# Optimization experiments

Hardware: AMD Instinct MI355X
Metric: run time of the kernel (lower is better)

Reference implementation:

```python
import jax, jax.numpy as jnp
import numpy as np

B, S, D, H = 4, 2048, 1024, 16
DH = D // H
SCALE = 1.0 / np.sqrt(DH).astype(np.float32)


def setup_inputs() -> dict:
    key = jax.random.key(0)
    k1, k2, k3 = jax.random.split(key, 3)
    x = jax.random.normal(k1, (B, S, D), dtype=jnp.float32)
    w_qkv = jax.random.normal(k2, (D, 3 * D), dtype=jnp.float32) * (1.0 / np.sqrt(D))
    b_qkv = jnp.zeros((3 * D,), dtype=jnp.float32)
    w_out = jax.random.normal(k3, (D, D), dtype=jnp.float32) * (1.0 / np.sqrt(D))
    b_out = jnp.zeros((D,), dtype=jnp.float32)
    return {"x": x, "w_qkv": w_qkv, "b_qkv": b_qkv, "w_out": w_out, "b_out": b_out}


def reference(x, w_qkv, b_qkv, w_out, b_out):
    b, s, d = x.shape
    qkv = x @ w_qkv + b_qkv                       # [b, s, 3d]
    qkv = qkv.reshape(b, s, 3, H, DH)
    qkv = jnp.transpose(qkv, (2, 0, 3, 1, 4))     # [3, b, h, s, dh]
    q, k, v = qkv[0], qkv[1], qkv[2]
    scores = jnp.einsum("bhqd,bhkd->bhqk", q, k) * SCALE
    weights = jax.nn.softmax(scores, axis=-1)
    attn = jnp.einsum("bhqk,bhkd->bhqd", weights, v)
    attn = jnp.transpose(attn, (0, 2, 1, 3)).reshape(b, s, d)
    return attn @ w_out + b_out
```

## Files before the change

kernel.cpp:

```cpp
#include <hip/hip_runtime.h>


typedef _Float16 f16;
typedef __attribute__((ext_vector_type(8))) _Float16 f16x8;
typedef __attribute__((ext_vector_type(4))) _Float16 f16x4;
typedef __attribute__((ext_vector_type(4))) float f32x4;
typedef __attribute__((ext_vector_type(16))) float f32x16;
typedef __attribute__((ext_vector_type(4))) unsigned u32x4;
typedef __attribute__((ext_vector_type(2))) int i32x2;

#define MFMA16F(a, b, c) __builtin_amdgcn_mfma_f32_16x16x32_f16((a), (b), (c), 0, 0, 0)
#define MFMA32F(a, b, c) __builtin_amdgcn_mfma_f32_32x32x16_f16((a), (b), (c), 0, 0, 0)

__device__ __forceinline__ i32x2 pl32_swap(unsigned a, unsigned b) {
  return __builtin_amdgcn_permlane32_swap((int)a, (int)b, false, false);
}

__device__ __forceinline__ void gload16(void* lds, const void* g) {
  __builtin_amdgcn_global_load_lds(
      (const __attribute__((address_space(1))) unsigned int*)g,
      (__attribute__((address_space(3))) unsigned int*)lds, 16, 0, 0);
}

__device__ __forceinline__ f16* lds_addr(f16* t, int row, int col) {
  return (f16*)((char*)t + row * 128 + ((col * 2) ^ ((row & 7) << 4)));
}
__device__ __forceinline__ f16x8 lds8(const f16* t, int row, int col) {
  return *(const f16x8*)lds_addr((f16*)t, row, col);
}

#define Q_PRESCALE 0.18033688011117f

__device__ __forceinline__ void transpose_tile(const float* __restrict__ in,
                                               f16* __restrict__ t_out, int R, int C,
                                               int bx, int by, int tid,
                                               float (*tile)[65]) {
  const int r0 = by * 64;
  const int c0 = bx * 64;
  const int lr = tid >> 4;
  const int lc = (tid & 15) * 4;
#pragma unroll
  for (int i = 0; i < 4; ++i) {
    float4 v = *(const float4*)&in[(size_t)(r0 + lr + i * 16) * C + c0 + lc];
    tile[lr + i * 16][lc] = v.x;
    tile[lr + i * 16][lc + 1] = v.y;
    tile[lr + i * 16][lc + 2] = v.z;
    tile[lr + i * 16][lc + 3] = v.w;
  }
  __syncthreads();
#pragma unroll
  for (int p = 0; p < 2; ++p) {
    const int id = p * 256 + tid;
    const int oc = id >> 3;
    const int orr = (id & 7) * 8;
    f16x8 h;
#pragma unroll
    for (int j = 0; j < 8; ++j) h[j] = (f16)tile[orr + j][oc];
    *(f16x8*)&t_out[(size_t)(c0 + oc) * R + r0 + orr] = h;
  }
}

__global__ __launch_bounds__(256) void prep_kernel(
    const float* __restrict__ x, f16* __restrict__ x_h,
    const float* __restrict__ w_qkv, f16* __restrict__ wqT_h,
    const float* __restrict__ w_out, f16* __restrict__ woT_h) {
  __shared__ float tile[64][65];
  const int b = blockIdx.x;
  const int tid = threadIdx.x;
  if (b < 4096) {
    const int idx = b * 2048 + tid * 8;
    float v[8];
    *(float4*)&v[0] = *(const float4*)&x[idx];
    *(float4*)&v[4] = *(const float4*)&x[idx + 4];
    f16x8 h;
#pragma unroll
    for (int j = 0; j < 8; ++j) h[j] = (f16)v[j];
    *(f16x8*)&x_h[idx] = h;
  } else if (b < 4864) {
    const int tb = b - 4096;
    transpose_tile(w_qkv, wqT_h, 1024, 3072, tb % 48, tb / 48, tid, tile);
  } else {
    const int tb = b - 4864;
    transpose_tile(w_out, woT_h, 1024, 1024, tb & 15, tb >> 4, tid, tile);
  }
}

template <int MODE>
__global__ __launch_bounds__(256, 2) void gemm_kernel(
    const f16* __restrict__ A, const f16* __restrict__ BT,
    const float* __restrict__ bias,
    f16* __restrict__ q_h, f16* __restrict__ k_h, f16* __restrict__ vt_h,
    float* __restrict__ C, int M, int N, int K) {
  __shared__ __align__(16) f16 As[2][128 * 64];
  __shared__ __align__(16) f16 Bs[2][128 * 64];

  const int tid = threadIdx.x;
  const int lane = tid & 63;
  const int wv = tid >> 6;
  const int lo16 = lane & 15;
  const int hi4 = lane >> 4;
  const int wr = wv >> 1;
  const int wc = wv & 1;
  const int m0 = blockIdx.y * 128;
  const int n0 = blockIdx.x * 128;

  f32x4 acc[4][4];
#pragma unroll
  for (int i = 0; i < 4; ++i)
#pragma unroll
    for (int j = 0; j < 4; ++j) acc[i][j] = (f32x4){0.f, 0.f, 0.f, 0.f};

  auto stage = [&](int buf, int kt) {
#pragma unroll
    for (int p = 0; p < 4; ++p) {
      const int cbase = p * 256 + wv * 64;
      const int c = cbase + lane;
      const int row = c >> 3;
      const int colc = (c & 7) ^ (row & 7);
      gload16(&As[buf][cbase * 8], &A[(size_t)(m0 + row) * K + kt + colc * 8]);
      gload16(&Bs[buf][cbase * 8], &BT[(size_t)(n0 + row) * K + kt + colc * 8]);
    }
  };

  auto compute = [&](const f16* Ac, const f16* Bc) {
#pragma unroll
    for (int ks = 0; ks < 2; ++ks) {
      f16x8 ah[4], bh[4];
#pragma unroll
      for (int t4 = 0; t4 < 4; ++t4) {
        ah[t4] = lds8((f16*)Ac, wr * 64 + t4 * 16 + lo16, ks * 32 + hi4 * 8);
        bh[t4] = lds8((f16*)Bc, wc * 64 + t4 * 16 + lo16, ks * 32 + hi4 * 8);
      }
      __builtin_amdgcn_s_setprio(1);
#pragma unroll
      for (int mt = 0; mt < 4; ++mt)
#pragma unroll
        for (int nt = 0; nt < 4; ++nt)
          acc[mt][nt] = MFMA16F(ah[mt], bh[nt], acc[mt][nt]);
      __builtin_amdgcn_s_setprio(0);
    }
  };

  stage(0, 0);
  __syncthreads();

  const int NT = K >> 6;
  for (int t = 0; t < NT; t += 2) {
    if (t + 1 < NT) stage(1, (t + 1) * 64);
    compute(As[0], Bs[0]);
    __syncthreads();
    if (t + 2 < NT) stage(0, (t + 2) * 64);
    compute(As[1], Bs[1]);
    __syncthreads();
  }

#pragma unroll
  for (int mt = 0; mt < 4; ++mt) {
    const int gmb = m0 + wr * 64 + mt * 16 + hi4 * 4;
#pragma unroll
    for (int nt = 0; nt < 4; ++nt) {
      const int gn = n0 + wc * 64 + nt * 16 + lo16;
      float v[4];
#pragma unroll
      for (int r = 0; r < 4; ++r) v[r] = acc[mt][nt][r] + bias[gn];
      if (MODE == 0) {
#pragma unroll
        for (int r = 0; r < 4; ++r) C[(size_t)(gmb + r) * N + gn] = v[r];
      } else {
        const int which = gn >> 10;
        const int h = (gn >> 6) & 15;
        const int dh = gn & 63;
        const int b = gmb >> 11;
        const int s = gmb & 2047;
        const size_t bh = (size_t)b * 16 + h;
        if (which == 0) {
#pragma unroll
          for (int r = 0; r < 4; ++r)
            q_h[(bh * 2048 + s + r) * 64 + dh] = (f16)(v[r] * Q_PRESCALE);
        } else if (which == 1) {
#pragma unroll
          for (int r = 0; r < 4; ++r)
            k_h[(bh * 2048 + s + r) * 64 + dh] = (f16)v[r];
        } else {
          f16x4 hh;
#pragma unroll
          for (int r = 0; r < 4; ++r) hh[r] = (f16)v[r];
          *(f16x4*)&vt_h[(bh * 64 + dh) * 2048 + s] = hh;
        }
      }
    }
  }
}

__global__ __launch_bounds__(256, 2) void attn_kernel(
    const f16* __restrict__ q_h, const f16* __restrict__ k_h,
    const f16* __restrict__ vt_h, f16* __restrict__ o) {
  __shared__ __align__(16) f16 Kh[2][64 * 64], Vh[2][64 * 64];

  const int tid = threadIdx.x;
  const int lane = tid & 63;
  const int wv = tid >> 6;
  const int l31 = lane & 31;
  const int h2 = lane >> 5;
  const int id0 = blockIdx.x;
  const int id = ((id0 & 7) << 6) | (id0 >> 3);
  const int bh = id >> 3;
  const int qb = id & 7;
  const size_t kvbase = (size_t)bh * 2048 * 64;
  const size_t vtbase = (size_t)bh * 64 * 2048;
  const int q0 = qb * 256 + wv * 64;

  const int c0idx = wv * 64 + lane;
  const int srow = c0idx >> 3;
  const int scol = ((c0idx & 7) ^ (srow & 7)) * 8;
  const int c1idx = 256 + wv * 64 + lane;
  const int srow1 = c1idx >> 3;
  const int scol1 = ((c1idx & 7) ^ (srow1 & 7)) * 8;

  auto stage = [&](int buf, int kv0) {
    gload16(&Kh[buf][(wv * 64) * 8], &k_h[kvbase + (size_t)(kv0 + srow) * 64 + scol]);
    gload16(&Vh[buf][(wv * 64) * 8], &vt_h[vtbase + (size_t)srow * 2048 + kv0 + scol]);
    gload16(&Kh[buf][(256 + wv * 64) * 8], &k_h[kvbase + (size_t)(kv0 + srow1) * 64 + scol1]);
    gload16(&Vh[buf][(256 + wv * 64) * 8], &vt_h[vtbase + (size_t)srow1 * 2048 + kv0 + scol1]);
  };

  f16x8 qh[2][4];
#pragma unroll
  for (int qs = 0; qs < 2; ++qs)
#pragma unroll
    for (int kt = 0; kt < 4; ++kt)
      qh[qs][kt] = *(const f16x8*)&q_h[kvbase + (size_t)(q0 + qs * 32 + l31) * 64 +
                                       kt * 16 + h2 * 8];

  const f16x8 ones = {(f16)1, (f16)1, (f16)1, (f16)1, (f16)1, (f16)1, (f16)1, (f16)1};

  f32x16 o_acc[2][2], acc_l[2];
#pragma unroll
  for (int qs = 0; qs < 2; ++qs)
#pragma unroll
    for (int i = 0; i < 16; ++i) {
      o_acc[qs][0][i] = 0.f;
      o_acc[qs][1][i] = 0.f;
      acc_l[qs][i] = 0.f;
    }

  auto tile_compute = [&](const f16* Kc, const f16* Vc) {
#pragma unroll
    for (int s = 0; s < 2; ++s) {
      f16x8 kb[4];
#pragma unroll
      for (int kt = 0; kt < 4; ++kt)
        kb[kt] = lds8((f16*)Kc, s * 32 + l31, kt * 16 + h2 * 8);

      f32x16 sa0, sa1;
#pragma unroll
      for (int i = 0; i < 16; ++i) {
        sa0[i] = 0.f;
        sa1[i] = 0.f;
      }
      __builtin_amdgcn_s_setprio(1);
#pragma unroll
      for (int kt = 0; kt < 4; ++kt) {
        sa0 = MFMA32F(kb[kt], qh[0][kt], sa0);
        sa1 = MFMA32F(kb[kt], qh[1][kt], sa1);
      }
      __builtin_amdgcn_s_setprio(0);

      f16x8 vb[2][2];
#pragma unroll
      for (int dt = 0; dt < 2; ++dt)
#pragma unroll
        for (int b = 0; b < 2; ++b)
          vb[dt][b] = lds8((f16*)Vc, dt * 32 + l31, s * 32 + b * 16 + h2 * 8);

#pragma unroll
      for (int qs = 0; qs < 2; ++qs) {
        const f32x16& sa = qs ? sa1 : sa0;
        unsigned w[8];
#pragma unroll
        for (int m = 0; m < 8; ++m) {
          const float pa_f = __builtin_amdgcn_exp2f(sa[2 * m]);
          const float pb_f = __builtin_amdgcn_exp2f(sa[2 * m + 1]);
          auto pk = __builtin_amdgcn_cvt_pkrtz(pa_f, pb_f);
          w[m] = __builtin_bit_cast(unsigned, pk);
        }
        f16x8 pa[2];
#pragma unroll
        for (int b = 0; b < 2; ++b) {
          const i32x2 r02 = pl32_swap(w[4 * b + 0], w[4 * b + 2]);
          const i32x2 r13 = pl32_swap(w[4 * b + 1], w[4 * b + 3]);
          u32x4 tw;
          tw[0] = (unsigned)r02[0];
          tw[1] = (unsigned)r13[0];
          tw[2] = (unsigned)r02[1];
          tw[3] = (unsigned)r13[1];
          pa[b] = __builtin_bit_cast(f16x8, tw);
        }
        __builtin_amdgcn_s_setprio(1);
#pragma unroll
        for (int b = 0; b < 2; ++b) {
          acc_l[qs] = MFMA32F(pa[b], ones, acc_l[qs]);
#pragma unroll
          for (int dt = 0; dt < 2; ++dt)
            o_acc[qs][dt] = MFMA32F(pa[b], vb[dt][b], o_acc[qs][dt]);
        }
        __builtin_amdgcn_s_setprio(0);
      }
    }
  };

  stage(0, 0);
  __syncthreads();

  for (int t = 0; t < 32; t += 2) {
    if (t + 1 < 32) stage(1, (t + 1) * 64);
    tile_compute(Kh[0], Vh[0]);
    __syncthreads();
    if (t + 2 < 32) stage(0, (t + 2) * 64);
    tile_compute(Kh[1], Vh[1]);
    __syncthreads();
  }

  const int b_ = bh >> 4;
  const int h_ = bh & 15;
#pragma unroll
  for (int qs = 0; qs < 2; ++qs)
#pragma unroll
    for (int dt = 0; dt < 2; ++dt)
#pragma unroll
      for (int r = 0; r < 16; ++r) {
        const int s_row = q0 + qs * 32 + (r & 3) + 8 * (r >> 2) + 4 * h2;
        const size_t idx =
            ((size_t)(b_ * 2048 + s_row)) * 1024 + h_ * 64 + dt * 32 + l31;
        o[idx] = (f16)(o_acc[qs][dt][r] / acc_l[qs][r]);
      }
}

extern "C" void kernel_launch(void* const* d_in, const int* in_sizes, int n_in,
                              void* d_out, int out_size, void* d_ws, size_t ws_size,
                              hipStream_t stream) {
  const float* x = (const float*)d_in[0];
  const float* w_qkv = (const float*)d_in[1];
  const float* b_qkv = (const float*)d_in[2];
  const float* w_out = (const float*)d_in[3];
  const float* b_out = (const float*)d_in[4];
  float* out = (float*)d_out;

  f16* ws = (f16*)d_ws;
  const size_t SZ = (size_t)64 * 2048 * 64;
  f16* q_h = ws;
  f16* k_h = ws + SZ;
  f16* vt_h = ws + 2 * SZ;
  f16* x_h = ws + 3 * SZ;
  f16* wqT_h = ws + 4 * SZ;
  f16* woT_h = wqT_h + (size_t)3072 * 1024;

  dim3 blk(256);
  prep_kernel<<<dim3(5120), blk, 0, stream>>>(x, x_h, w_qkv, wqT_h, w_out, woT_h);

  gemm_kernel<1><<<dim3(24, 64), blk, 0, stream>>>(
      x_h, wqT_h, b_qkv, q_h, k_h, vt_h, nullptr, 8192, 3072, 1024);

  attn_kernel<<<dim3(512), blk, 0, stream>>>(q_h, k_h, vt_h, x_h);

  gemm_kernel<0><<<dim3(8, 64), blk, 0, stream>>>(
      x_h, woT_h, b_out, nullptr, nullptr, nullptr, out, 8192, 1024, 1024);
}
```

Baseline: 186.7 us.

## Split attention KV range in two halves and combine partials in separate kernel

```diff
diff --git a/kernel.cpp b/kernel.cpp
--- a/kernel.cpp
+++ b/kernel.cpp
@@ -192,9 +192,9 @@
   }
 }
 
-__global__ __launch_bounds__(256, 2) void attn_kernel(
+__global__ __launch_bounds__(256, 2) void attn_partial_kernel(
     const f16* __restrict__ q_h, const f16* __restrict__ k_h,
-    const f16* __restrict__ vt_h, f16* __restrict__ o) {
+    const f16* __restrict__ vt_h, f16* __restrict__ po, float* __restrict__ lw) {
   __shared__ __align__(16) f16 Kh[2][64 * 64], Vh[2][64 * 64];
 
   const int tid = threadIdx.x;
@@ -203,12 +203,14 @@
   const int l31 = lane & 31;
   const int h2 = lane >> 5;
   const int id0 = blockIdx.x;
-  const int id = ((id0 & 7) << 6) | (id0 >> 3);
-  const int bh = id >> 3;
+  const int id = ((id0 & 7) << 7) | (id0 >> 3);
+  const int bh = id >> 4;
+  const int half = (id >> 3) & 1;
   const int qb = id & 7;
   const size_t kvbase = (size_t)bh * 2048 * 64;
   const size_t vtbase = (size_t)bh * 64 * 2048;
   const int q0 = qb * 256 + wv * 64;
+  const int base_kv = half * 1024;
 
   const int c0idx = wv * 64 + lane;
   const int srow = c0idx >> 3;
@@ -309,31 +311,60 @@
     }
   };
 
-  stage(0, 0);
+  stage(0, base_kv);
   __syncthreads();
 
-  for (int t = 0; t < 32; t += 2) {
-    if (t + 1 < 32) stage(1, (t + 1) * 64);
+  for (int t = 0; t < 16; t += 2) {
+    if (t + 1 < 16) stage(1, base_kv + (t + 1) * 64);
     tile_compute(Kh[0], Vh[0]);
     __syncthreads();
-    if (t + 2 < 32) stage(0, (t + 2) * 64);
+    if (t + 2 < 16) stage(0, base_kv + (t + 2) * 64);
     tile_compute(Kh[1], Vh[1]);
     __syncthreads();
   }
 
-  const int b_ = bh >> 4;
-  const int h_ = bh & 15;
-#pragma unroll
-  for (int qs = 0; qs < 2; ++qs)
+  f16* po_out = po + (size_t)half * 8388608;
+  float* l_out = lw + (size_t)half * 131072;
+#pragma unroll
+  for (int qs = 0; qs < 2; ++qs) {
 #pragma unroll
     for (int dt = 0; dt < 2; ++dt)
 #pragma unroll
       for (int r = 0; r < 16; ++r) {
-        const int s_row = q0 + qs * 32 + (r & 3) + 8 * (r >> 2) + 4 * h2;
-        const size_t idx =
-            ((size_t)(b_ * 2048 + s_row)) * 1024 + h_ * 64 + dt * 32 + l31;
-        o[idx] = (f16)(o_acc[qs][dt][r] / acc_l[qs][r]);
-      }
+        const int q = q0 + qs * 32 + (r & 3) + 8 * (r >> 2) + 4 * h2;
+        po_out[((size_t)bh * 2048 + q) * 64 + dt * 32 + l31] = (f16)o_acc[qs][dt][r];
+      }
+    if (l31 == 0) {
+#pragma unroll
+      for (int r = 0; r < 16; ++r) {
+        const int q = q0 + qs * 32 + (r & 3) + 8 * (r >> 2) + 4 * h2;
+        l_out[bh * 2048 + q] = acc_l[qs][r];
+      }
+    }
+  }
+}
+
+__global__ __launch_bounds__(256) void combine_kernel(
+    const f16* __restrict__ po, const float* __restrict__ lw,
+    f16* __restrict__ o) {
+  const int n = 1048576;
+  int c = blockIdx.x * 256 + threadIdx.x;
+  const int stride = gridDim.x * 256;
+  for (; c < n; c += stride) {
+    const int q = c >> 3;
+    const int g = c & 7;
+    const float inv = 1.0f / (lw[q] + lw[131072 + q]);
+    f16x8 a = *(const f16x8*)&po[(size_t)q * 64 + g * 8];
+    f16x8 b = *(const f16x8*)&po[8388608 + (size_t)q * 64 + g * 8];
+    f16x8 r;
+#pragma unroll
+    for (int j = 0; j < 8; ++j) r[j] = (f16)(((float)a[j] + (float)b[j]) * inv);
+    const int bh = q >> 11;
+    const int s = q & 2047;
+    const int b_ = bh >> 4;
+    const int h_ = bh & 15;
+    *(f16x8*)&o[((size_t)(b_ * 2048 + s)) * 1024 + h_ * 64 + g * 8] = r;
+  }
 }
 
 extern "C" void kernel_launch(void* const* d_in, const int* in_sizes, int n_in,
@@ -354,6 +385,8 @@
   f16* x_h = ws + 3 * SZ;
   f16* wqT_h = ws + 4 * SZ;
   f16* woT_h = wqT_h + (size_t)3072 * 1024;
+  f16* po = woT_h + (size_t)1024 * 1024;
+  float* lw = (float*)(po + 2 * SZ);
 
   dim3 blk(256);
   prep_kernel<<<dim3(5120), blk, 0, stream>>>(x, x_h, w_qkv, wqT_h, w_out, woT_h);
@@ -361,7 +394,9 @@
   gemm_kernel<1><<<dim3(24, 64), blk, 0, stream>>>(
       x_h, wqT_h, b_qkv, q_h, k_h, vt_h, nullptr, 8192, 3072, 1024);
 
-  attn_kernel<<<dim3(512), blk, 0, stream>>>(q_h, k_h, vt_h, x_h);
+  attn_partial_kernel<<<dim3(1024), blk, 0, stream>>>(q_h, k_h, vt_h, po, lw);
+
+  combine_kernel<<<dim3(2048), blk, 0, stream>>>(po, lw, x_h);
 
   gemm_kernel<0><<<dim3(8, 64), blk, 0, stream>>>(
       x_h, woT_h, b_out, nullptr, nullptr, nullptr, out, 8192, 1024, 1024);
```

New measurement: 193.3 us. 1.04x slower.
